# Kernel optimization log

Measured on AMD Instinct MI355X. Metric: run time of the kernel, lower is better.

Reference implementation:

```python
import jax, jax.numpy as jnp
import numpy as np

B, N, F_IN, D, K, INTER = 64, 512, 128, 128, 32, 256
EPS = 1e-5


def _bn(x, g, b, axes):
    # BatchNorm in training mode (biased batch statistics), matching torch BN forward
    m = x.mean(axis=axes, keepdims=True)
    v = x.var(axis=axes, keepdims=True)
    return (x - m) * jax.lax.rsqrt(v + EPS) * g + b


def setup_inputs() -> dict:
    key = jax.random.key(0)
    ks = jax.random.split(key, 12)
    u = lambda k, s: jax.random.uniform(k, s, jnp.float32, -0.3, 0.3)
    return {
        "data": jax.random.normal(ks[0], (B, N, F_IN), jnp.float32),
        "emb_weight": u(ks[1], (N, D)),          # nn.Embedding(node_num, dim), kaiming-uniform-ish
        "lin_W": u(ks[2], (F_IN, D)),            # GraphLayer lin (no bias)
        "att_i": u(ks[3], (D,)),
        "att_j": u(ks[4], (D,)),
        "att_em_i": u(ks[5], (D,)),
        "att_em_j": u(ks[6], (D,)),
        "gnn_bias": jnp.zeros((D,), jnp.float32),
        "gnn_bn_g": jnp.ones((D,), jnp.float32),
        "gnn_bn_b": jnp.zeros((D,), jnp.float32),
        "bn_out_g": jnp.ones((D,), jnp.float32),
        "bn_out_b": jnp.zeros((D,), jnp.float32),
        "W1": u(ks[7], (D, INTER)), "b1": jnp.zeros((INTER,), jnp.float32),
        "bn1_g": jnp.ones((INTER,), jnp.float32), "bn1_b": jnp.zeros((INTER,), jnp.float32),
        "W2": u(ks[8], (INTER, INTER)), "b2": jnp.zeros((INTER,), jnp.float32),
        "bn2_g": jnp.ones((INTER,), jnp.float32), "bn2_b": jnp.zeros((INTER,), jnp.float32),
        "W3": u(ks[9], (INTER, 1)), "b3": jnp.zeros((1,), jnp.float32),
    }


def reference(data, emb_weight, lin_W, att_i, att_j, att_em_i, att_em_j,
              gnn_bias, gnn_bn_g, gnn_bn_b, bn_out_g, bn_out_b,
              W1, b1, bn1_g, bn1_b, W2, b2, bn2_g, bn2_b, W3, b3):
    M = B * N
    x = data.reshape(M, F_IN)

    # --- learned graph: cosine similarity + topk over DETACHED embeddings ---
    w = jax.lax.stop_gradient(emb_weight)
    nrm = jnp.linalg.norm(w, axis=-1)
    cos = (w @ w.T) / (nrm[:, None] * nrm[None, :])
    topk_idx = jax.lax.top_k(cos, K)[1]                    # [N, K]

    # gated_edge_index = (j=topk neighbor as source, i as target), tiled per batch
    src0 = topk_idx.reshape(-1)                            # [N*K] sources (j)
    dst0 = jnp.repeat(jnp.arange(N), K)                    # [N*K] targets (i)
    off = (jnp.arange(B) * N)[:, None]
    src = (src0[None, :] + off).reshape(-1)                # [B*N*K]
    dst = (dst0[None, :] + off).reshape(-1)
    valid = src != dst                                     # remove_self_loops
    loops = jnp.arange(M)                                  # add_self_loops
    src = jnp.concatenate([src, loops])
    dst = jnp.concatenate([dst, loops])
    valid = jnp.concatenate([valid, jnp.ones((M,), bool)])

    # --- GraphLayer (GAT-style, heads=1, concat=False) ---
    x_lin = x @ lin_W                                      # [M, D]
    emb_b = jnp.tile(emb_weight, (B, 1))                   # [M, D] embedding repeated per batch
    # per-node score halves; gather scalars at edges instead of [E, 2D] keys
    s_i = x_lin @ att_i + emb_b @ att_em_i                 # key_i . cat(att_i, att_em_i)
    s_j = x_lin @ att_j + emb_b @ att_em_j
    logit = jax.nn.leaky_relu(s_i[dst] + s_j[src], 0.2)    # [E]
    logit = jnp.where(valid, logit, -1e9)                  # removed self-edges contribute 0
    mx = jax.ops.segment_max(logit, dst, num_segments=M)
    e = jnp.where(valid, jnp.exp(logit - mx[dst]), 0.0)
    den = jax.ops.segment_sum(e, dst, num_segments=M)
    alpha = e / den[dst]                                   # softmax over incoming edges
    agg = jax.ops.segment_sum(x_lin[src] * alpha[:, None], dst, num_segments=M)
    gcn = jax.nn.relu(_bn(agg + gnn_bias, gnn_bn_g, gnn_bn_b, (0,)))  # GNNLayer bn+relu

    # --- gating by embedding, BN over channel dim, OutLayer MLP ---
    h = gcn.reshape(B, N, D) * emb_weight[None]            # [B, N, D]
    h = jax.nn.relu(_bn(h, bn_out_g, bn_out_b, (0, 1)))    # BatchNorm1d over D channels
    # dropout p=0.2 is identity in eval mode
    o = jax.nn.relu(_bn(h @ W1 + b1, bn1_g, bn1_b, (0, 1)))
    o = jax.nn.relu(_bn(o @ W2 + b2, bn2_g, bn2_b, (0, 1)))
    o = (o @ W3 + b3).reshape(B, N)                        # out.view(-1, node_num)
    return o
```

## Files before the change

### kernel.cpp

```cpp
#include <hip/hip_runtime.h>
#include <math.h>

#define M_ROWS 32768
#define NNODES 512
#define KNBR   32
#define EPSBN  1e-5f

typedef __bf16 bf16x8 __attribute__((ext_vector_type(8)));
typedef __bf16 bf16x4 __attribute__((ext_vector_type(4)));
typedef __bf16 bf16x2 __attribute__((ext_vector_type(2)));
typedef float  f32x4  __attribute__((ext_vector_type(4)));

#if defined(__has_builtin)
#if __has_builtin(__builtin_amdgcn_global_load_lds)
#define HAVE_GLL 1
#endif
#endif

__device__ __forceinline__ void async_ld16(void* lds, const void* g){
#ifdef HAVE_GLL
    __builtin_amdgcn_global_load_lds((__attribute__((address_space(1))) void*)(g),
                                     (__attribute__((address_space(3))) void*)(lds),
                                     16, 0, 0);
#else
    *(bf16x8*)lds = *(const bf16x8*)g;
#endif
}

__global__ __launch_bounds__(256) void setup_kernel(
    const float* __restrict__ emb,
    const float* __restrict__ aei, const float* __restrict__ aej,
    const float* __restrict__ lin_W, const float* __restrict__ W1,
    const float* __restrict__ W2,
    int* __restrict__ topk, float* __restrict__ e_i, float* __restrict__ e_j,
    __bf16* __restrict__ Wp0, __bf16* __restrict__ Wp1, __bf16* __restrict__ Wp2,
    float* __restrict__ stats)
{
    int bid = blockIdx.x, tid = threadIdx.x;
    if (bid >= 512){
        if (bid == 568){
            for (int i = tid; i < 1536; i += 256) stats[i] = 0.f;
            return;
        }
        int gidx = (bid - 512)*256 + tid;
        const float* W; __bf16* o; int C, lg;
        if (gidx < 2048)      { W = lin_W; o = Wp0; C = 128; lg = gidx; }
        else if (gidx < 6144) { W = W1;    o = Wp1; C = 256; lg = gidx - 2048; }
        else                  { W = W2;    o = Wp2; C = 256; lg = gidx - 6144; }
        int kg = (C == 128) ? (lg >> 7) : (lg >> 8);
        int c  = lg & (C - 1);
        bf16x8 pk;
        #pragma unroll
        for (int j = 0; j < 8; ++j) pk[j] = (__bf16)W[(size_t)(kg*8 + j)*C + c];
        *(bf16x8*)&o[(size_t)lg*8] = pk;
        return;
    }

    __shared__ float wi[128];
    __shared__ float cosv[512];
    int i = bid;
    if (tid < 128) wi[tid] = emb[i*128 + tid];
    __syncthreads();
    float ni = 0.f;
    #pragma unroll 8
    for (int d = 0; d < 128; ++d) ni += wi[d]*wi[d];
    float rni = sqrtf(ni);
    for (int jj = tid; jj < 512; jj += 256){
        const float4* wj4 = (const float4*)(emb + jj*128);
        float dot = 0.f, nj = 0.f;
        #pragma unroll 8
        for (int d4 = 0; d4 < 32; ++d4){
            float4 w = wj4[d4];
            dot += wi[4*d4+0]*w.x + wi[4*d4+1]*w.y + wi[4*d4+2]*w.z + wi[4*d4+3]*w.w;
            nj  += w.x*w.x + w.y*w.y + w.z*w.z + w.w*w.w;
        }
        cosv[jj] = dot / (rni * sqrtf(nj));
    }
    __syncthreads();
    if (tid < 64){
        int lane = tid;
        float v[8];
        #pragma unroll
        for (int jj = 0; jj < 8; ++jj) v[jj] = cosv[lane + 64*jj];
        for (int k = 0; k < KNBR; ++k){
            float bv = v[0]; int bj = 0;
            #pragma unroll
            for (int jj = 1; jj < 8; ++jj) if (v[jj] > bv){ bv = v[jj]; bj = jj; }
            int bi = lane + 64*bj;
            #pragma unroll
            for (int mask = 1; mask < 64; mask <<= 1){
                float ov = __shfl_xor(bv, mask);
                int   oi = __shfl_xor(bi, mask);
                if (ov > bv || (ov == bv && oi < bi)){ bv = ov; bi = oi; }
            }
            if (lane == 0) topk[i*KNBR + k] = bi;
            if ((bi & 63) == lane){
                int jj = bi >> 6;
                #pragma unroll
                for (int j2 = 0; j2 < 8; ++j2) if (j2 == jj) v[j2] = -2e30f;
            }
        }
    } else if (tid < 128){
        int lane = tid - 64;
        float ai = wi[lane]*aei[lane] + wi[lane+64]*aei[lane+64];
        float aj = wi[lane]*aej[lane] + wi[lane+64]*aej[lane+64];
        for (int off = 32; off; off >>= 1){
            ai += __shfl_down(ai, off);
            aj += __shfl_down(aj, off);
        }
        if (lane == 0){ e_i[i] = ai; e_j[i] = aj; }
    }
}

__global__ __launch_bounds__(256) void xlin_gemm_kernel(
    const float* __restrict__ A,
    const __bf16* __restrict__ Wp,
    const float* __restrict__ att_i, const float* __restrict__ att_j,
    const float* __restrict__ e_i,   const float* __restrict__ e_j,
    __bf16* __restrict__ outp,
    float* __restrict__ s_i, float* __restrict__ s_j)
{
    __shared__ __align__(16) __bf16 As[64][136];
    __shared__ __align__(16) __bf16 Bp[16][128][8];

    int tid  = threadIdx.x;
    int lane = tid & 63, wv = tid >> 6;
    int mrow = lane & 15, q = lane >> 4;
    int row0 = blockIdx.x * 64;

    f32x4 acc[8];
    #pragma unroll
    for (int ct = 0; ct < 8; ++ct) acc[ct] = (f32x4){0.f,0.f,0.f,0.f};

    #pragma unroll
    for (int i = 0; i < 8; ++i){
        int p = tid + i*256;
        const __bf16* src = Wp + ((size_t)(p>>7)*128 + (p&127))*8;
        async_ld16((__bf16*)Bp + (size_t)p*8, src);
    }
    #pragma unroll
    for (int i = 0; i < 4; ++i){
        int p = tid + i*256;
        int r = p >> 4, c8 = p & 15;
        const float* src = &A[(size_t)(row0 + r)*128 + c8*8];
        float4 a0 = *(const float4*)src;
        float4 a1 = *(const float4*)(src + 4);
        bf16x8 o;
        o[0]=(__bf16)a0.x; o[1]=(__bf16)a0.y; o[2]=(__bf16)a0.z; o[3]=(__bf16)a0.w;
        o[4]=(__bf16)a1.x; o[5]=(__bf16)a1.y; o[6]=(__bf16)a1.z; o[7]=(__bf16)a1.w;
        *(bf16x8*)&As[r][c8*8] = o;
    }
    __syncthreads();

    #pragma unroll
    for (int ks = 0; ks < 4; ++ks){
        bf16x8 a = *(const bf16x8*)&As[wv*16 + mrow][ks*32 + q*8];
        #pragma unroll
        for (int ct = 0; ct < 8; ++ct){
            bf16x8 bb = *(const bf16x8*)&Bp[ks*4 + q][ct*16 + mrow][0];
            acc[ct] = __builtin_amdgcn_mfma_f32_16x16x32_bf16(a, bb, acc[ct], 0, 0, 0);
        }
    }

    float ai[4] = {0,0,0,0}, aj[4] = {0,0,0,0};
    #pragma unroll
    for (int ct = 0; ct < 8; ++ct){
        int col = ct*16 + mrow;
        float wti = att_i[col], wtj = att_j[col];
        #pragma unroll
        for (int reg = 0; reg < 4; ++reg){
            int row = row0 + wv*16 + q*4 + reg;
            float v = acc[ct][reg];
            outp[(size_t)row*128 + col] = (__bf16)v;
            ai[reg] += v*wti; aj[reg] += v*wtj;
        }
    }
    #pragma unroll
    for (int mask = 1; mask < 16; mask <<= 1){
        #pragma unroll
        for (int reg = 0; reg < 4; ++reg){
            ai[reg] += __shfl_xor(ai[reg], mask);
            aj[reg] += __shfl_xor(aj[reg], mask);
        }
    }
    if (mrow == 0){
        #pragma unroll
        for (int reg = 0; reg < 4; ++reg){
            int row = row0 + wv*16 + q*4 + reg;
            int n = row & 511;
            s_i[row] = ai[reg] + e_i[n];
            s_j[row] = aj[reg] + e_j[n];
        }
    }
}

template<bool GATE>
__global__ __launch_bounds__(256) void gemm2_kernel(
    const __bf16* __restrict__ A, int a_stride, int Ktot,
    const float* __restrict__ st1, const float* __restrict__ g1, const float* __restrict__ b1,
    const float* __restrict__ emb,
    const float* __restrict__ st2, const float* __restrict__ g2, const float* __restrict__ b2,
    const __bf16* __restrict__ Wp, int Ctot,
    const float* __restrict__ bias,
    __bf16* __restrict__ outp,
    float* __restrict__ outstats, int outK)
{
    __shared__ __align__(16) __bf16 As[128][136];
    __shared__ __align__(16) __bf16 Bp[16][128][8];
    __shared__ float nsc1[128], nsh1[128], nsc2[128], nsh2[128];
    __shared__ float statS[128], statQ[128];

    int tid  = threadIdx.x;
    int lane = tid & 63, wv = tid >> 6;
    int mrow = lane & 15, q = lane >> 4;
    int cb0  = blockIdx.y * 128;
    int row0 = blockIdx.x * 128;

    f32x4 acc[2][8];
    #pragma unroll
    for (int rt = 0; rt < 2; ++rt)
        #pragma unroll
        for (int ct = 0; ct < 8; ++ct)
            acc[rt][ct] = (f32x4){0.f,0.f,0.f,0.f};

    for (int kc = 0; kc < Ktot; kc += 128){
        if (tid < 128){
            int f = kc + tid;
            float mean = st1[f] * (1.f/32768.f);
            float var  = st1[Ktot + f] * (1.f/32768.f) - mean*mean;
            float sc   = g1[f] / sqrtf(var + EPSBN);
            nsc1[tid] = sc;
            nsh1[tid] = b1[f] - mean*sc;
            if (GATE){
                float mean2 = st2[tid] * (1.f/32768.f);
                float var2  = st2[128 + tid] * (1.f/32768.f) - mean2*mean2;
                float sc2   = g2[tid] / sqrtf(var2 + EPSBN);
                nsc2[tid] = sc2;
                nsh2[tid] = b2[tid] - mean2*sc2;
            }
        }
        __syncthreads();

        int kg0 = kc >> 3;
        #pragma unroll
        for (int i = 0; i < 8; ++i){
            int p = tid + i*256;
            const __bf16* src = Wp + ((size_t)(kg0 + (p>>7))*Ctot + cb0 + (p&127))*8;
            async_ld16((__bf16*)Bp + (size_t)p*8, src);
        }
        #pragma unroll
        for (int i = 0; i < 8; ++i){
            int p = tid + i*256;
            int r = p >> 4, c8 = p & 15;
            bf16x8 v = *(const bf16x8*)&A[(size_t)(row0 + r)*a_stride + kc + c8*8];
            bf16x8 o;
            if (GATE){
                const float* ep = &emb[(size_t)((row0 + r) & 511)*128 + c8*8];
                float4 e0 = *(const float4*)ep;
                float4 e1 = *(const float4*)(ep + 4);
                float ee[8] = {e0.x,e0.y,e0.z,e0.w,e1.x,e1.y,e1.z,e1.w};
                #pragma unroll
                for (int j = 0; j < 8; ++j){
                    int f = c8*8 + j;
                    float hv = fmaxf((float)v[j]*nsc1[f] + nsh1[f], 0.f) * ee[j];
                    o[j] = (__bf16)fmaxf(hv*nsc2[f] + nsh2[f], 0.f);
                }
            } else {
                #pragma unroll
                for (int j = 0; j < 8; ++j){
                    int f = c8*8 + j;
                    o[j] = (__bf16)fmaxf((float)v[j]*nsc1[f] + nsh1[f], 0.f);
                }
            }
            *(bf16x8*)&As[r][c8*8] = o;
        }
        __syncthreads();

        #pragma unroll
        for (int ks = 0; ks < 4; ++ks){
            bf16x8 a0 = *(const bf16x8*)&As[wv*32      + mrow][ks*32 + q*8];
            bf16x8 a1 = *(const bf16x8*)&As[wv*32 + 16 + mrow][ks*32 + q*8];
            #pragma unroll
            for (int ct = 0; ct < 8; ++ct){
                bf16x8 bb = *(const bf16x8*)&Bp[ks*4 + q][ct*16 + mrow][0];
                acc[0][ct] = __builtin_amdgcn_mfma_f32_16x16x32_bf16(a0, bb, acc[0][ct], 0, 0, 0);
                acc[1][ct] = __builtin_amdgcn_mfma_f32_16x16x32_bf16(a1, bb, acc[1][ct], 0, 0, 0);
            }
        }
        __syncthreads();
    }

    if (tid < 128){ statS[tid] = 0.f; statQ[tid] = 0.f; }
    __syncthreads();

    float cs[8] = {0,0,0,0,0,0,0,0}, cq[8] = {0,0,0,0,0,0,0,0};
    #pragma unroll
    for (int ct = 0; ct < 8; ++ct){
        int col = cb0 + ct*16 + mrow;
        float bv = bias[col];
        #pragma unroll
        for (int rt = 0; rt < 2; ++rt){
            #pragma unroll
            for (int reg = 0; reg < 4; ++reg){
                int row = row0 + wv*32 + rt*16 + q*4 + reg;
                __bf16 bvv = (__bf16)(acc[rt][ct][reg] + bv);
                outp[(size_t)row*Ctot + col] = bvv;
                float fv = (float)bvv; cs[ct] += fv; cq[ct] += fv*fv;
            }
        }
    }
    #pragma unroll
    for (int ct = 0; ct < 8; ++ct){
        float s  = cs[ct]; s  += __shfl_xor(s, 16);  s  += __shfl_xor(s, 32);
        float qq = cq[ct]; qq += __shfl_xor(qq, 16); qq += __shfl_xor(qq, 32);
        if (q == 0){
            atomicAdd(&statS[ct*16 + mrow], s);
            atomicAdd(&statQ[ct*16 + mrow], qq);
        }
    }
    __syncthreads();
    if (tid < 128){
        atomicAdd(&outstats[cb0 + tid],        statS[tid]);
        atomicAdd(&outstats[outK + cb0 + tid], statQ[tid]);
    }
}

__global__ __launch_bounds__(256) void agg_kernel(const __bf16* __restrict__ xl,
                                                  const float* __restrict__ s_i,
                                                  const float* __restrict__ s_j,
                                                  const int* __restrict__ topk,
                                                  const float2* __restrict__ gnn_bias2,
                                                  __bf16* __restrict__ aggp){
    int gid  = blockIdx.x*256 + threadIdx.x;
    int m    = gid >> 6, lane = gid & 63;
    int b = m >> 9, i = m & 511;
    int src; bool valid;
    if (lane < KNBR){ int j = topk[i*KNBR + lane]; src = (b << 9) + j; valid = (j != i); }
    else            { src = m; valid = (lane == KNBR); }
    float l = s_i[m] + s_j[src];
    l = (l >= 0.f) ? l : 0.2f*l;
    l = valid ? l : -1e30f;
    float mx = l;
    #pragma unroll
    for (int mask = 1; mask < 64; mask <<= 1) mx = fmaxf(mx, __shfl_xor(mx, mask));
    float e = valid ? __expf(l - mx) : 0.f;
    float den = e;
    #pragma unroll
    for (int mask = 1; mask < 64; mask <<= 1) den += __shfl_xor(den, mask);
    float alpha = e / den;

    float2 acc = make_float2(0.f, 0.f);
    #pragma unroll 4
    for (int k = 0; k < 33; ++k){
        float a = __shfl(alpha, k);
        int   s = __shfl(src, k);
        bf16x2 v = *(const bf16x2*)&xl[(size_t)s*128 + lane*2];
        acc.x += a*(float)v[0]; acc.y += a*(float)v[1];
    }
    float2 bv = gnn_bias2[lane];
    bf16x2 o;
    o[0] = (__bf16)(acc.x + bv.x);
    o[1] = (__bf16)(acc.y + bv.y);
    *(bf16x2*)&aggp[(size_t)m*128 + lane*2] = o;
}

__global__ __launch_bounds__(256) void colstats_kernel(const __bf16* __restrict__ X,
                                                       float* __restrict__ st){
    int tid = threadIdx.x;
    int cg = tid & 31, rs = tid >> 5;
    int c0 = cg*4;
    float s[4] = {0,0,0,0}, qq[4] = {0,0,0,0};
    for (int m = blockIdx.x*8 + rs; m < M_ROWS; m += gridDim.x*8){
        bf16x4 v = *(const bf16x4*)&X[(size_t)m*128 + c0];
        #pragma unroll
        for (int j = 0; j < 4; ++j){ float f = (float)v[j]; s[j] += f; qq[j] += f*f; }
    }
    __shared__ float rS[8][128], rQ[8][128];
    #pragma unroll
    for (int j = 0; j < 4; ++j){ rS[rs][c0+j] = s[j]; rQ[rs][c0+j] = qq[j]; }
    __syncthreads();
    if (tid < 128){
        float ts = 0.f, tq = 0.f;
        #pragma unroll
        for (int u = 0; u < 8; ++u){ ts += rS[u][tid]; tq += rQ[u][tid]; }
        atomicAdd(&st[tid],       ts);
        atomicAdd(&st[128 + tid], tq);
    }
}

__global__ __launch_bounds__(256) void hstats_kernel(const __bf16* __restrict__ agg,
                                                     const float* __restrict__ gst,
                                                     const float* __restrict__ g,
                                                     const float* __restrict__ bta,
                                                     const float* __restrict__ emb,
                                                     float* __restrict__ hstats){
    int tid = threadIdx.x;
    int cg = tid & 31, rs = tid >> 5;
    int c0 = cg*4;
    float sc[4], sh[4];
    #pragma unroll
    for (int j = 0; j < 4; ++j){
        float mean = gst[c0+j] * (1.f/32768.f);
        float var  = gst[128 + c0+j] * (1.f/32768.f) - mean*mean;
        sc[j] = g[c0+j] / sqrtf(var + EPSBN);
        sh[j] = bta[c0+j] - mean*sc[j];
    }
    float s[4] = {0,0,0,0}, qq[4] = {0,0,0,0};
    for (int m = blockIdx.x*8 + rs; m < M_ROWS; m += gridDim.x*8){
        bf16x4 v = *(const bf16x4*)&agg[(size_t)m*128 + c0];
        float4 e = *(const float4*)&emb[(size_t)(m & 511)*128 + c0];
        float f0 = fmaxf((float)v[0]*sc[0] + sh[0], 0.f) * e.x;
        float f1 = fmaxf((float)v[1]*sc[1] + sh[1], 0.f) * e.y;
        float f2 = fmaxf((float)v[2]*sc[2] + sh[2], 0.f) * e.z;
        float f3 = fmaxf((float)v[3]*sc[3] + sh[3], 0.f) * e.w;
        s[0]+=f0; qq[0]+=f0*f0; s[1]+=f1; qq[1]+=f1*f1;
        s[2]+=f2; qq[2]+=f2*f2; s[3]+=f3; qq[3]+=f3*f3;
    }
    __shared__ float rS[8][128], rQ[8][128];
    #pragma unroll
    for (int j = 0; j < 4; ++j){ rS[rs][c0+j] = s[j]; rQ[rs][c0+j] = qq[j]; }
    __syncthreads();
    if (tid < 128){
        float ts = 0.f, tq = 0.f;
        #pragma unroll
        for (int u = 0; u < 8; ++u){ ts += rS[u][tid]; tq += rQ[u][tid]; }
        atomicAdd(&hstats[tid],       ts);
        atomicAdd(&hstats[128 + tid], tq);
    }
}

__global__ __launch_bounds__(256) void final_kernel(const __bf16* __restrict__ t2,
                                                    const float* __restrict__ st,
                                                    const float* __restrict__ g,
                                                    const float* __restrict__ bta,
                                                    const float* __restrict__ W3,
                                                    const float* __restrict__ b3,
                                                    float* __restrict__ outp){
    int gid = blockIdx.x*256 + threadIdx.x;
    int wid = gid >> 6, lane = gid & 63;
    int c0 = lane*4;
    bf16x4 v  = *(const bf16x4*)&t2[(size_t)wid*256 + c0];
    float4 w3 = *(const float4*)&W3[c0];
    float4 gg = *(const float4*)&g[c0];
    float4 bb = *(const float4*)&bta[c0];
    float4 sm = *(const float4*)&st[c0];
    float4 sq = *(const float4*)&st[256 + c0];
    float accv = 0.f;
    {
        float mean, var, val;
        mean = sm.x*(1.f/32768.f); var = sq.x*(1.f/32768.f) - mean*mean;
        val = ((float)v[0]-mean)*(gg.x/sqrtf(var+EPSBN)) + bb.x; accv += fmaxf(val,0.f)*w3.x;
        mean = sm.y*(1.f/32768.f); var = sq.y*(1.f/32768.f) - mean*mean;
        val = ((float)v[1]-mean)*(gg.y/sqrtf(var+EPSBN)) + bb.y; accv += fmaxf(val,0.f)*w3.y;
        mean = sm.z*(1.f/32768.f); var = sq.z*(1.f/32768.f) - mean*mean;
        val = ((float)v[2]-mean)*(gg.z/sqrtf(var+EPSBN)) + bb.z; accv += fmaxf(val,0.f)*w3.z;
        mean = sm.w*(1.f/32768.f); var = sq.w*(1.f/32768.f) - mean*mean;
        val = ((float)v[3]-mean)*(gg.w/sqrtf(var+EPSBN)) + bb.w; accv += fmaxf(val,0.f)*w3.w;
    }
    for (int off = 32; off; off >>= 1) accv += __shfl_down(accv, off);
    if (lane == 0) outp[wid] = accv + b3[0];
}

extern "C" void kernel_launch(void* const* d_in, const int* in_sizes, int n_in,
                              void* d_out, int out_size, void* d_ws, size_t ws_size,
                              hipStream_t stream)
{
    (void)in_sizes; (void)n_in; (void)out_size; (void)ws_size;
    const float* data   = (const float*)d_in[0];
    const float* emb    = (const float*)d_in[1];
    const float* lin_W  = (const float*)d_in[2];
    const float* att_i  = (const float*)d_in[3];
    const float* att_j  = (const float*)d_in[4];
    const float* aem_i  = (const float*)d_in[5];
    const float* aem_j  = (const float*)d_in[6];
    const float* gnn_bias = (const float*)d_in[7];
    const float* gnn_g  = (const float*)d_in[8];
    const float* gnn_b  = (const float*)d_in[9];
    const float* bno_g  = (const float*)d_in[10];
    const float* bno_b  = (const float*)d_in[11];
    const float* W1     = (const float*)d_in[12];
    const float* b1     = (const float*)d_in[13];
    const float* bn1_g  = (const float*)d_in[14];
    const float* bn1_b  = (const float*)d_in[15];
    const float* W2     = (const float*)d_in[16];
    const float* b2     = (const float*)d_in[17];
    const float* bn2_g  = (const float*)d_in[18];
    const float* bn2_b  = (const float*)d_in[19];
    const float* W3     = (const float*)d_in[20];
    const float* b3     = (const float*)d_in[21];
    float* outp = (float*)d_out;
    char*  ws   = (char*)d_ws;

    int*    topk     = (int*)ws;
    float*  e_i      = (float*)(ws + 65536);
    float*  e_j      = (float*)(ws + 67584);
    float*  s_i      = (float*)(ws + 69632);
    float*  s_j      = (float*)(ws + 200704);
    float*  stats    = (float*)(ws + 331776);
    float*  gnnstats = stats;
    float*  hstats   = stats + 256;
    float*  bn1stats = stats + 512;
    float*  bn2stats = stats + 1024;
    __bf16* Wp0      = (__bf16*)(ws + 337920);
    __bf16* Wp1      = (__bf16*)(ws + 370688);
    __bf16* Wp2      = (__bf16*)(ws + 436224);
    __bf16* xlin     = (__bf16*)(ws + 1048576);
    __bf16* aggb     = (__bf16*)(ws + 1048576 +   8388608);
    __bf16* t1       = (__bf16*)(ws + 1048576 + 2*8388608);
    __bf16* t2       = (__bf16*)(ws + 1048576 + 2*8388608 + 16777216);

    setup_kernel<<<569, 256, 0, stream>>>(emb, aem_i, aem_j, lin_W, W1, W2,
                                          topk, e_i, e_j, Wp0, Wp1, Wp2, stats);

    xlin_gemm_kernel<<<512, 256, 0, stream>>>(data, Wp0, att_i, att_j, e_i, e_j,
                                              xlin, s_i, s_j);

    agg_kernel<<<M_ROWS/4, 256, 0, stream>>>(xlin, s_i, s_j, topk,
                                             (const float2*)gnn_bias, aggb);
    colstats_kernel<<<256, 256, 0, stream>>>(aggb, gnnstats);
    hstats_kernel<<<256, 256, 0, stream>>>(aggb, gnnstats, gnn_g, gnn_b, emb, hstats);

    gemm2_kernel<true><<<dim3(256,2), 256, 0, stream>>>(
        aggb, 128, 128, gnnstats, gnn_g, gnn_b, emb, hstats, bno_g, bno_b,
        Wp1, 256, b1, t1, bn1stats, 256);

    gemm2_kernel<false><<<dim3(256,2), 256, 0, stream>>>(
        t1, 256, 256, bn1stats, bn1_g, bn1_b, nullptr, nullptr, nullptr, nullptr,
        Wp2, 256, b2, t2, bn2stats, 256);

    final_kernel<<<M_ROWS/4, 256, 0, stream>>>(t2, bn2stats, bn2_g, bn2_b, W3, b3, outp);
}
```

Baseline: 259.6 us.

## Fuse x_lin GEMM into setup, fold BN stats into aggregation, retile gemm2

Merges the topk/setup kernel and the x_lin GEMM into one launch. GEMM blocks convert lin_W to bf16 in-block instead of reading a pre-packed copy, and the per-node embedding attention terms move to a small separate kernel that agg adds in. The aggregation kernel now processes 8 rows per wave and accumulates the GNN BatchNorm column sums with atomics, so the separate colstats pass over agg is gone. gemm2 changes its warp tiling from 32x128 to 64x64 per wave for better operand reuse. The cost is redundant lin_W conversion in every GEMM block, a larger shared-memory footprint, and more atomics.

```diff
diff --git a/kernel.cpp b/kernel.cpp
--- a/kernel.cpp
+++ b/kernel.cpp
@@ -27,38 +27,114 @@
 #endif
 }
 
-__global__ __launch_bounds__(256) void setup_kernel(
-    const float* __restrict__ emb,
-    const float* __restrict__ aei, const float* __restrict__ aej,
+__global__ __launch_bounds__(256) void k1_kernel(
+    const float* __restrict__ data, const float* __restrict__ emb,
     const float* __restrict__ lin_W, const float* __restrict__ W1,
     const float* __restrict__ W2,
-    int* __restrict__ topk, float* __restrict__ e_i, float* __restrict__ e_j,
-    __bf16* __restrict__ Wp0, __bf16* __restrict__ Wp1, __bf16* __restrict__ Wp2,
-    float* __restrict__ stats)
+    const float* __restrict__ att_i, const float* __restrict__ att_j,
+    int* __restrict__ topk,
+    __bf16* __restrict__ Wp1, __bf16* __restrict__ Wp2,
+    float* __restrict__ stats,
+    __bf16* __restrict__ xlin, float* __restrict__ s_i, float* __restrict__ s_j)
 {
+    __shared__ __align__(16) char sm[50176];
     int bid = blockIdx.x, tid = threadIdx.x;
-    if (bid >= 512){
-        if (bid == 568){
+
+    if (bid < 512){
+        __bf16 (*As)[136] = (__bf16(*)[136])sm;
+        bf16x8* Bp = (bf16x8*)(sm + 17408);
+        int lane = tid & 63, wv = tid >> 6;
+        int mrow = lane & 15, q = lane >> 4;
+        int row0 = bid * 64;
+
+        #pragma unroll
+        for (int i = 0; i < 8; ++i){
+            int g = tid + i*256;
+            int kg = g >> 7, c = g & 127;
+            bf16x8 pk;
+            #pragma unroll
+            for (int j = 0; j < 8; ++j) pk[j] = (__bf16)lin_W[(size_t)(kg*8 + j)*128 + c];
+            Bp[g] = pk;
+        }
+        #pragma unroll
+        for (int i = 0; i < 4; ++i){
+            int p = tid + i*256;
+            int r = p >> 4, c8 = p & 15;
+            const float* src = &data[(size_t)(row0 + r)*128 + c8*8];
+            float4 a0 = *(const float4*)src;
+            float4 a1 = *(const float4*)(src + 4);
+            bf16x8 o;
+            o[0]=(__bf16)a0.x; o[1]=(__bf16)a0.y; o[2]=(__bf16)a0.z; o[3]=(__bf16)a0.w;
+            o[4]=(__bf16)a1.x; o[5]=(__bf16)a1.y; o[6]=(__bf16)a1.z; o[7]=(__bf16)a1.w;
+            *(bf16x8*)&As[r][c8*8] = o;
+        }
+        __syncthreads();
+
+        f32x4 acc[8];
+        #pragma unroll
+        for (int ct = 0; ct < 8; ++ct) acc[ct] = (f32x4){0.f,0.f,0.f,0.f};
+        #pragma unroll
+        for (int ks = 0; ks < 4; ++ks){
+            bf16x8 a = *(const bf16x8*)&As[wv*16 + mrow][ks*32 + q*8];
+            #pragma unroll
+            for (int ct = 0; ct < 8; ++ct){
+                bf16x8 bb = Bp[(ks*4 + q)*128 + ct*16 + mrow];
+                acc[ct] = __builtin_amdgcn_mfma_f32_16x16x32_bf16(a, bb, acc[ct], 0, 0, 0);
+            }
+        }
+
+        float ai[4] = {0,0,0,0}, aj[4] = {0,0,0,0};
+        #pragma unroll
+        for (int ct = 0; ct < 8; ++ct){
+            int col = ct*16 + mrow;
+            float wti = att_i[col], wtj = att_j[col];
+            #pragma unroll
+            for (int reg = 0; reg < 4; ++reg){
+                int row = row0 + wv*16 + q*4 + reg;
+                float v = acc[ct][reg];
+                xlin[(size_t)row*128 + col] = (__bf16)v;
+                ai[reg] += v*wti; aj[reg] += v*wtj;
+            }
+        }
+        #pragma unroll
+        for (int mask = 1; mask < 16; mask <<= 1){
+            #pragma unroll
+            for (int reg = 0; reg < 4; ++reg){
+                ai[reg] += __shfl_xor(ai[reg], mask);
+                aj[reg] += __shfl_xor(aj[reg], mask);
+            }
+        }
+        if (mrow == 0){
+            #pragma unroll
+            for (int reg = 0; reg < 4; ++reg){
+                int row = row0 + wv*16 + q*4 + reg;
+                s_i[row] = ai[reg];
+                s_j[row] = aj[reg];
+            }
+        }
+        return;
+    }
+
+    if (bid >= 1024){
+        if (bid == 1072){
             for (int i = tid; i < 1536; i += 256) stats[i] = 0.f;
             return;
         }
-        int gidx = (bid - 512)*256 + tid;
-        const float* W; __bf16* o; int C, lg;
-        if (gidx < 2048)      { W = lin_W; o = Wp0; C = 128; lg = gidx; }
-        else if (gidx < 6144) { W = W1;    o = Wp1; C = 256; lg = gidx - 2048; }
-        else                  { W = W2;    o = Wp2; C = 256; lg = gidx - 6144; }
-        int kg = (C == 128) ? (lg >> 7) : (lg >> 8);
-        int c  = lg & (C - 1);
+        int gidx = (bid - 1024)*256 + tid;
+        const float* W; __bf16* o; int lg;
+        if (gidx < 4096){ W = W1; o = Wp1; lg = gidx; }
+        else            { W = W2; o = Wp2; lg = gidx - 4096; }
+        int kg = lg >> 8, c = lg & 255;
         bf16x8 pk;
         #pragma unroll
-        for (int j = 0; j < 8; ++j) pk[j] = (__bf16)W[(size_t)(kg*8 + j)*C + c];
+        for (int j = 0; j < 8; ++j) pk[j] = (__bf16)W[(size_t)(kg*8 + j)*256 + c];
         *(bf16x8*)&o[(size_t)lg*8] = pk;
         return;
     }
 
-    __shared__ float wi[128];
-    __shared__ float cosv[512];
-    int i = bid;
+    float* wi   = (float*)sm;
+    float* cosv = (float*)(sm + 512);
+    int i = bid - 512;
     if (tid < 128) wi[tid] = emb[i*128 + tid];
     __syncthreads();
     float ni = 0.f;
@@ -100,97 +176,90 @@
                 for (int j2 = 0; j2 < 8; ++j2) if (j2 == jj) v[j2] = -2e30f;
             }
         }
-    } else if (tid < 128){
-        int lane = tid - 64;
-        float ai = wi[lane]*aei[lane] + wi[lane+64]*aei[lane+64];
-        float aj = wi[lane]*aej[lane] + wi[lane+64]*aej[lane+64];
+    }
+}
+
+__global__ __launch_bounds__(256) void agg_kernel(const __bf16* __restrict__ xl,
+                                                  const float* __restrict__ s_i,
+                                                  const float* __restrict__ s_j,
+                                                  const float* __restrict__ emb,
+                                                  const float* __restrict__ aei,
+                                                  const float* __restrict__ aej,
+                                                  const int* __restrict__ topk,
+                                                  const float2* __restrict__ gnn_bias2,
+                                                  __bf16* __restrict__ aggp,
+                                                  float* __restrict__ gnnstats){
+    int tid = threadIdx.x;
+    int wv = tid >> 6, lane = tid & 63;
+    int gw = blockIdx.x*4 + wv;
+    float2 bv = gnn_bias2[lane];
+
+    float s0 = 0.f, s1 = 0.f, q0 = 0.f, q1 = 0.f;
+
+    #pragma unroll 1
+    for (int u = 0; u < 8; ++u){
+        int m = gw*8 + u;
+        int b = m >> 9, i = m & 511;
+        int src; bool valid;
+        if (lane < KNBR){ int j = topk[i*KNBR + lane]; src = (b << 9) + j; valid = (j != i); }
+        else            { src = m; valid = (lane == KNBR); }
+        float l = s_i[m] + aei[i] + s_j[src] + aej[src & 511];
+        l = (l >= 0.f) ? l : 0.2f*l;
+        l = valid ? l : -1e30f;
+        float mx = l;
+        #pragma unroll
+        for (int mask = 1; mask < 64; mask <<= 1) mx = fmaxf(mx, __shfl_xor(mx, mask));
+        float e = valid ? __expf(l - mx) : 0.f;
+        float den = e;
+        #pragma unroll
+        for (int mask = 1; mask < 64; mask <<= 1) den += __shfl_xor(den, mask);
+        float alpha = e / den;
+
+        float2 acc = make_float2(0.f, 0.f);
+        #pragma unroll 4
+        for (int k = 0; k < 33; ++k){
+            float a = __shfl(alpha, k);
+            int   s = __shfl(src, k);
+            bf16x2 v = *(const bf16x2*)&xl[(size_t)s*128 + lane*2];
+            acc.x += a*(float)v[0]; acc.y += a*(float)v[1];
+        }
+        bf16x2 o;
+        o[0] = (__bf16)(acc.x + bv.x);
+        o[1] = (__bf16)(acc.y + bv.y);
+        *(bf16x2*)&aggp[(size_t)m*128 + lane*2] = o;
+        float r0 = (float)o[0], r1 = (float)o[1];
+        s0 += r0; q0 += r0*r0; s1 += r1; q1 += r1*r1;
+    }
+
+    __shared__ float rS[4][128], rQ[4][128];
+    rS[wv][lane*2]   = s0; rS[wv][lane*2+1] = s1;
+    rQ[wv][lane*2]   = q0; rQ[wv][lane*2+1] = q1;
+    __syncthreads();
+    if (tid < 128){
+        float ts = rS[0][tid] + rS[1][tid] + rS[2][tid] + rS[3][tid];
+        float tq = rQ[0][tid] + rQ[1][tid] + rQ[2][tid] + rQ[3][tid];
+        atomicAdd(&gnnstats[tid],       ts);
+        atomicAdd(&gnnstats[128 + tid], tq);
+    }
+}
+
+__global__ __launch_bounds__(256) void escore_kernel(const float* __restrict__ emb,
+                                                     const float* __restrict__ aem_i,
+                                                     const float* __restrict__ aem_j,
+                                                     float* __restrict__ e_i,
+                                                     float* __restrict__ e_j){
+    int tid = threadIdx.x;
+    int wid = tid >> 6, lane = tid & 63;
+    for (int n = blockIdx.x*4 + wid; n < NNODES; n += gridDim.x*4){
+        const float* w = emb + (size_t)n*128;
+        float ai = w[lane]*aem_i[lane] + w[lane+64]*aem_i[lane+64];
+        float aj = w[lane]*aem_j[lane] + w[lane+64]*aem_j[lane+64];
+        #pragma unroll
         for (int off = 32; off; off >>= 1){
             ai += __shfl_down(ai, off);
             aj += __shfl_down(aj, off);
         }
-        if (lane == 0){ e_i[i] = ai; e_j[i] = aj; }
-    }
-}
-
-__global__ __launch_bounds__(256) void xlin_gemm_kernel(
-    const float* __restrict__ A,
-    const __bf16* __restrict__ Wp,
-    const float* __restrict__ att_i, const float* __restrict__ att_j,
-    const float* __restrict__ e_i,   const float* __restrict__ e_j,
-    __bf16* __restrict__ outp,
-    float* __restrict__ s_i, float* __restrict__ s_j)
-{
-    __shared__ __align__(16) __bf16 As[64][136];
-    __shared__ __align__(16) __bf16 Bp[16][128][8];
-
-    int tid  = threadIdx.x;
-    int lane = tid & 63, wv = tid >> 6;
-    int mrow = lane & 15, q = lane >> 4;
-    int row0 = blockIdx.x * 64;
-
-    f32x4 acc[8];
-    #pragma unroll
-    for (int ct = 0; ct < 8; ++ct) acc[ct] = (f32x4){0.f,0.f,0.f,0.f};
-
-    #pragma unroll
-    for (int i = 0; i < 8; ++i){
-        int p = tid + i*256;
-        const __bf16* src = Wp + ((size_t)(p>>7)*128 + (p&127))*8;
-        async_ld16((__bf16*)Bp + (size_t)p*8, src);
-    }
-    #pragma unroll
-    for (int i = 0; i < 4; ++i){
-        int p = tid + i*256;
-        int r = p >> 4, c8 = p & 15;
-        const float* src = &A[(size_t)(row0 + r)*128 + c8*8];
-        float4 a0 = *(const float4*)src;
-        float4 a1 = *(const float4*)(src + 4);
-        bf16x8 o;
-        o[0]=(__bf16)a0.x; o[1]=(__bf16)a0.y; o[2]=(__bf16)a0.z; o[3]=(__bf16)a0.w;
-        o[4]=(__bf16)a1.x; o[5]=(__bf16)a1.y; o[6]=(__bf16)a1.z; o[7]=(__bf16)a1.w;
-        *(bf16x8*)&As[r][c8*8] = o;
-    }
-    __syncthreads();
-
-    #pragma unroll
-    for (int ks = 0; ks < 4; ++ks){
-        bf16x8 a = *(const bf16x8*)&As[wv*16 + mrow][ks*32 + q*8];
-        #pragma unroll
-        for (int ct = 0; ct < 8; ++ct){
-            bf16x8 bb = *(const bf16x8*)&Bp[ks*4 + q][ct*16 + mrow][0];
-            acc[ct] = __builtin_amdgcn_mfma_f32_16x16x32_bf16(a, bb, acc[ct], 0, 0, 0);
-        }
-    }
-
-    float ai[4] = {0,0,0,0}, aj[4] = {0,0,0,0};
-    #pragma unroll
-    for (int ct = 0; ct < 8; ++ct){
-        int col = ct*16 + mrow;
-        float wti = att_i[col], wtj = att_j[col];
-        #pragma unroll
-        for (int reg = 0; reg < 4; ++reg){
-            int row = row0 + wv*16 + q*4 + reg;
-            float v = acc[ct][reg];
-            outp[(size_t)row*128 + col] = (__bf16)v;
-            ai[reg] += v*wti; aj[reg] += v*wtj;
-        }
-    }
-    #pragma unroll
-    for (int mask = 1; mask < 16; mask <<= 1){
-        #pragma unroll
-        for (int reg = 0; reg < 4; ++reg){
-            ai[reg] += __shfl_xor(ai[reg], mask);
-            aj[reg] += __shfl_xor(aj[reg], mask);
-        }
-    }
-    if (mrow == 0){
-        #pragma unroll
-        for (int reg = 0; reg < 4; ++reg){
-            int row = row0 + wv*16 + q*4 + reg;
-            int n = row & 511;
-            s_i[row] = ai[reg] + e_i[n];
-            s_j[row] = aj[reg] + e_j[n];
-        }
+        if (lane == 0){ e_i[n] = ai; e_j[n] = aj; }
     }
 }
 
@@ -213,14 +282,15 @@
     int tid  = threadIdx.x;
     int lane = tid & 63, wv = tid >> 6;
     int mrow = lane & 15, q = lane >> 4;
+    int wvr = wv & 1, wvc = wv >> 1;
     int cb0  = blockIdx.y * 128;
     int row0 = blockIdx.x * 128;
 
-    f32x4 acc[2][8];
+    f32x4 acc[4][4];
     #pragma unroll
-    for (int rt = 0; rt < 2; ++rt)
-        #pragma unroll
-        for (int ct = 0; ct < 8; ++ct)
+    for (int rt = 0; rt < 4; ++rt)
+        #pragma unroll
+        for (int ct = 0; ct < 4; ++ct)
             acc[rt][ct] = (f32x4){0.f,0.f,0.f,0.f};
 
     for (int kc = 0; kc < Ktot; kc += 128){
@@ -278,13 +348,16 @@
 
         #pragma unroll
         for (int ks = 0; ks < 4; ++ks){
-            bf16x8 a0 = *(const bf16x8*)&As[wv*32      + mrow][ks*32 + q*8];
-            bf16x8 a1 = *(const bf16x8*)&As[wv*32 + 16 + mrow][ks*32 + q*8];
-            #pragma unroll
-            for (int ct = 0; ct < 8; ++ct){
-                bf16x8 bb = *(const bf16x8*)&Bp[ks*4 + q][ct*16 + mrow][0];
-                acc[0][ct] = __builtin_amdgcn_mfma_f32_16x16x32_bf16(a0, bb, acc[0][ct], 0, 0, 0);
-                acc[1][ct] = __builtin_amdgcn_mfma_f32_16x16x32_bf16(a1, bb, acc[1][ct], 0, 0, 0);
+            bf16x8 a[4];
+            #pragma unroll
+            for (int rt = 0; rt < 4; ++rt)
+                a[rt] = *(const bf16x8*)&As[wvr*64 + rt*16 + mrow][ks*32 + q*8];
+            #pragma unroll
+            for (int ct = 0; ct < 4; ++ct){
+                bf16x8 bb = *(const bf16x8*)&Bp[ks*4 + q][wvc*64 + ct*16 + mrow][0];
+                #pragma unroll
+                for (int rt = 0; rt < 4; ++rt)
+                    acc[rt][ct] = __builtin_amdgcn_mfma_f32_16x16x32_bf16(a[rt], bb, acc[rt][ct], 0, 0, 0);
             }
         }
         __syncthreads();
@@ -293,98 +366,36 @@
     if (tid < 128){ statS[tid] = 0.f; statQ[tid] = 0.f; }
     __syncthreads();
 
-    float cs[8] = {0,0,0,0,0,0,0,0}, cq[8] = {0,0,0,0,0,0,0,0};
+    float cs[4] = {0,0,0,0}, cq[4] = {0,0,0,0};
     #pragma unroll
-    for (int ct = 0; ct < 8; ++ct){
-        int col = cb0 + ct*16 + mrow;
-        float bv = bias[col];
-        #pragma unroll
-        for (int rt = 0; rt < 2; ++rt){
+    for (int ct = 0; ct < 4; ++ct){
+        int lcol = wvc*64 + ct*16 + mrow;
+        int col  = cb0 + lcol;
+        float bvv = bias[col];
+        #pragma unroll
+        for (int rt = 0; rt < 4; ++rt){
             #pragma unroll
             for (int reg = 0; reg < 4; ++reg){
-                int row = row0 + wv*32 + rt*16 + q*4 + reg;
-                __bf16 bvv = (__bf16)(acc[rt][ct][reg] + bv);
-                outp[(size_t)row*Ctot + col] = bvv;
-                float fv = (float)bvv; cs[ct] += fv; cq[ct] += fv*fv;
+                int row = row0 + wvr*64 + rt*16 + q*4 + reg;
+                __bf16 ov = (__bf16)(acc[rt][ct][reg] + bvv);
+                outp[(size_t)row*Ctot + col] = ov;
+                float fv = (float)ov; cs[ct] += fv; cq[ct] += fv*fv;
             }
         }
     }
     #pragma unroll
-    for (int ct = 0; ct < 8; ++ct){
+    for (int ct = 0; ct < 4; ++ct){
         float s  = cs[ct]; s  += __shfl_xor(s, 16);  s  += __shfl_xor(s, 32);
         float qq = cq[ct]; qq += __shfl_xor(qq, 16); qq += __shfl_xor(qq, 32);
         if (q == 0){
-            atomicAdd(&statS[ct*16 + mrow], s);
-            atomicAdd(&statQ[ct*16 + mrow], qq);
+            atomicAdd(&statS[wvc*64 + ct*16 + mrow], s);
+            atomicAdd(&statQ[wvc*64 + ct*16 + mrow], qq);
         }
     }
     __syncthreads();
     if (tid < 128){
         atomicAdd(&outstats[cb0 + tid],        statS[tid]);
         atomicAdd(&outstats[outK + cb0 + tid], statQ[tid]);
-    }
-}
-
-__global__ __launch_bounds__(256) void agg_kernel(const __bf16* __restrict__ xl,
-                                                  const float* __restrict__ s_i,
-                                                  const float* __restrict__ s_j,
-                                                  const int* __restrict__ topk,
-                                                  const float2* __restrict__ gnn_bias2,
-                                                  __bf16* __restrict__ aggp){
-    int gid  = blockIdx.x*256 + threadIdx.x;
-    int m    = gid >> 6, lane = gid & 63;
-    int b = m >> 9, i = m & 511;
-    int src; bool valid;
-    if (lane < KNBR){ int j = topk[i*KNBR + lane]; src = (b << 9) + j; valid = (j != i); }
-    else            { src = m; valid = (lane == KNBR); }
-    float l = s_i[m] + s_j[src];
-    l = (l >= 0.f) ? l : 0.2f*l;
-    l = valid ? l : -1e30f;
-    float mx = l;
-    #pragma unroll
-    for (int mask = 1; mask < 64; mask <<= 1) mx = fmaxf(mx, __shfl_xor(mx, mask));
-    float e = valid ? __expf(l - mx) : 0.f;
-    float den = e;
-    #pragma unroll
-    for (int mask = 1; mask < 64; mask <<= 1) den += __shfl_xor(den, mask);
-    float alpha = e / den;
-
-    float2 acc = make_float2(0.f, 0.f);
-    #pragma unroll 4
-    for (int k = 0; k < 33; ++k){
-        float a = __shfl(alpha, k);
-        int   s = __shfl(src, k);
-        bf16x2 v = *(const bf16x2*)&xl[(size_t)s*128 + lane*2];
-        acc.x += a*(float)v[0]; acc.y += a*(float)v[1];
-    }
-    float2 bv = gnn_bias2[lane];
-    bf16x2 o;
-    o[0] = (__bf16)(acc.x + bv.x);
-    o[1] = (__bf16)(acc.y + bv.y);
-    *(bf16x2*)&aggp[(size_t)m*128 + lane*2] = o;
-}
-
-__global__ __launch_bounds__(256) void colstats_kernel(const __bf16* __restrict__ X,
-                                                       float* __restrict__ st){
-    int tid = threadIdx.x;
-    int cg = tid & 31, rs = tid >> 5;
-    int c0 = cg*4;
-    float s[4] = {0,0,0,0}, qq[4] = {0,0,0,0};
-    for (int m = blockIdx.x*8 + rs; m < M_ROWS; m += gridDim.x*8){
-        bf16x4 v = *(const bf16x4*)&X[(size_t)m*128 + c0];
-        #pragma unroll
-        for (int j = 0; j < 4; ++j){ float f = (float)v[j]; s[j] += f; qq[j] += f*f; }
-    }
-    __shared__ float rS[8][128], rQ[8][128];
-    #pragma unroll
-    for (int j = 0; j < 4; ++j){ rS[rs][c0+j] = s[j]; rQ[rs][c0+j] = qq[j]; }
-    __syncthreads();
-    if (tid < 128){
-        float ts = 0.f, tq = 0.f;
-        #pragma unroll
-        for (int u = 0; u < 8; ++u){ ts += rS[u][tid]; tq += rQ[u][tid]; }
-        atomicAdd(&st[tid],       ts);
-        atomicAdd(&st[128 + tid], tq);
     }
 }
 
@@ -501,23 +512,21 @@
     float*  hstats   = stats + 256;
     float*  bn1stats = stats + 512;
     float*  bn2stats = stats + 1024;
-    __bf16* Wp0      = (__bf16*)(ws + 337920);
-    __bf16* Wp1      = (__bf16*)(ws + 370688);
-    __bf16* Wp2      = (__bf16*)(ws + 436224);
+    __bf16* Wp1      = (__bf16*)(ws + 337920);
+    __bf16* Wp2      = (__bf16*)(ws + 403456);
     __bf16* xlin     = (__bf16*)(ws + 1048576);
     __bf16* aggb     = (__bf16*)(ws + 1048576 +   8388608);
     __bf16* t1       = (__bf16*)(ws + 1048576 + 2*8388608);
     __bf16* t2       = (__bf16*)(ws + 1048576 + 2*8388608 + 16777216);
 
-    setup_kernel<<<569, 256, 0, stream>>>(emb, aem_i, aem_j, lin_W, W1, W2,
-                                          topk, e_i, e_j, Wp0, Wp1, Wp2, stats);
-
-    xlin_gemm_kernel<<<512, 256, 0, stream>>>(data, Wp0, att_i, att_j, e_i, e_j,
-                                              xlin, s_i, s_j);
-
-    agg_kernel<<<M_ROWS/4, 256, 0, stream>>>(xlin, s_i, s_j, topk,
-                                             (const float2*)gnn_bias, aggb);
-    colstats_kernel<<<256, 256, 0, stream>>>(aggb, gnnstats);
+    escore_kernel<<<8, 256, 0, stream>>>(emb, aem_i, aem_j, e_i, e_j);
+
+    k1_kernel<<<1073, 256, 0, stream>>>(data, emb, lin_W, W1, W2, att_i, att_j,
+                                        topk, Wp1, Wp2, stats, xlin, s_i, s_j);
+
+    agg_kernel<<<1024, 256, 0, stream>>>(xlin, s_i, s_j, emb, e_i, e_j, topk,
+                                         (const float2*)gnn_bias, aggb, gnnstats);
+
     hstats_kernel<<<256, 256, 0, stream>>>(aggb, gnnstats, gnn_g, gnn_b, emb, hstats);
 
     gemm2_kernel<true><<<dim3(256,2), 256, 0, stream>>>(
```

Measured after the change: 282.1 us. 1.09x slower.
